# Optimization experiments

Hardware: AMD Instinct MI355X
Metric: run time of the kernel (lower is better)

The kernel has to match this reference:

```python
import jax, jax.numpy as jnp
import numpy as np
import math

PI = math.pi
PHI = (1.0 + math.sqrt(5.0)) / 2.0
D_MODEL = 1024
N_HEADS = 16
D_HEAD = D_MODEL // N_HEADS
LAYER_DEPTH = 0.5
LAYER_INDEX = 0
CONV_RATE = 0.1


def setup_inputs() -> dict:
    key = jax.random.key(0)
    ks = jax.random.split(key, 5)
    B, T = 2, 2048
    x = jax.random.normal(ks[0], (B, T, D_MODEL), dtype=jnp.float32)
    s = 1.0 / math.sqrt(D_MODEL)
    Wq = jax.random.normal(ks[1], (D_MODEL, D_MODEL), dtype=jnp.float32) * s
    Wk = jax.random.normal(ks[2], (D_MODEL, D_MODEL), dtype=jnp.float32) * s
    Wv = jax.random.normal(ks[3], (D_MODEL, D_MODEL), dtype=jnp.float32) * s
    We = jax.random.normal(ks[4], (D_MODEL, D_MODEL), dtype=jnp.float32) * s
    # per-head chamber init, matching ApertureChamber / _head_depth
    frac = jnp.arange(N_HEADS, dtype=jnp.float32) / max(N_HEADS - 1, 1)
    lo = LAYER_DEPTH * 0.5
    hi = 0.5 + LAYER_DEPTH * 0.5
    depth = lo + frac * (hi - lo)
    beta = 0.5 + 0.2 * (1.0 - 2.0 * depth)           # [H] raw (pre-sigmoid) params
    input_valve = jnp.full((N_HEADS,), 0.5, dtype=jnp.float32)
    output_valve = jnp.full((N_HEADS,), 0.5, dtype=jnp.float32)
    chi = jnp.ones((N_HEADS,), dtype=jnp.float32)
    return {"x": x, "Wq": Wq, "Wk": Wk, "Wv": Wv, "We": We,
            "beta": beta, "input_valve": input_valve,
            "output_valve": output_valve, "chi": chi}


def reference(x, Wq, Wk, Wv, We, beta, input_valve, output_valve, chi):
    B, T, D = x.shape
    H, dh = N_HEADS, D // N_HEADS
    conv_factor = 1.0 / PHI ** (LAYER_INDEX * CONV_RATE)
    scale = math.sqrt(dh * conv_factor)
    # QKV projections (torch Linear: x @ W.T), split heads -> [B,H,T,dh]
    q = (x @ Wq.T).reshape(B, T, H, dh).transpose(0, 2, 1, 3)
    k = (x @ Wk.T).reshape(B, T, H, dh).transpose(0, 2, 1, 3)
    v = (x @ Wv.T).reshape(B, T, H, dh).transpose(0, 2, 1, 3)
    attn = jax.nn.softmax(jnp.einsum('bhqd,bhkd->bhqk', q, k) / scale, axis=-1)
    converged = jnp.einsum('bhqk,bhkd->bhqd', attn, v)  # [B,H,T,dh]
    # ApertureChamber per head, vectorized over H (broadcast [H] -> [1,H,1,1])
    b = jax.nn.sigmoid(beta)[None, :, None, None]
    iv = jax.nn.sigmoid(input_valve)[None, :, None, None]
    ov = jax.nn.sigmoid(output_valve)[None, :, None, None]
    g = jnp.tanh(chi)[None, :, None, None]
    ang = PI * b
    ca, sa = jnp.cos(ang), jnp.sin(ang)
    x_in = converged * iv
    half = dh // 2  # d_head even -> no leftover lane
    xr, xi = x_in[..., :half], x_in[..., half:]
    rot = jnp.concatenate([xr * ca - xi * sa, xr * sa + xi * ca], axis=-1)
    out = rot * ov * g  # output valve + tanh(chi) gate
    combined = out.transpose(0, 2, 1, 3).reshape(B, T, D)
    return combined @ We.T
```

## Files before the change

### kernel.cpp

```cpp
#include <hip/hip_runtime.h>
#include <hip/hip_bf16.h>
#include <math.h>

typedef __bf16 bf16;
typedef __bf16 bf16x4 __attribute__((ext_vector_type(4)));
typedef __bf16 bf16x8 __attribute__((ext_vector_type(8)));
typedef float f32x4 __attribute__((ext_vector_type(4)));
typedef float f32x16 __attribute__((ext_vector_type(16)));
typedef unsigned int u32x4 __attribute__((ext_vector_type(4)));

static __device__ __forceinline__ f32x4 mfma16(bf16x8 a, bf16x8 b, f32x4 c) {
  return __builtin_amdgcn_mfma_f32_16x16x32_bf16(a, b, c, 0, 0, 0);
}
static __device__ __forceinline__ f32x16 mfma32(bf16x8 a, bf16x8 b, f32x16 c) {
  return __builtin_amdgcn_mfma_f32_32x32x16_bf16(a, b, c, 0, 0, 0);
}
static __device__ __forceinline__ void gld_lds16(const void* g, void* l) {
  __builtin_amdgcn_global_load_lds(
      (const __attribute__((address_space(1))) void*)g,
      (__attribute__((address_space(3))) void*)l, 16, 0, 0);
}
static __device__ __forceinline__ unsigned cvt_pk_bf16(float lo, float hi) {
  unsigned r;
  asm("v_cvt_pk_bf16_f32 %0, %1, %2" : "=v"(r) : "v"(lo), "v"(hi));
  return r;
}
static __device__ __forceinline__ float rsum16(f32x16 v) {
  float a0 = v[0] + v[8],  a1 = v[1] + v[9];
  float a2 = v[2] + v[10], a3 = v[3] + v[11];
  float a4 = v[4] + v[12], a5 = v[5] + v[13];
  float a6 = v[6] + v[14], a7 = v[7] + v[15];
  a0 += a4; a1 += a5; a2 += a6; a3 += a7;
  return (a0 + a1) + (a2 + a3);
}

__global__ void cast_all(const float* __restrict__ x, const float* __restrict__ Wq,
                         const float* __restrict__ Wk, const float* __restrict__ Wv,
                         const float* __restrict__ We,
                         bf16* __restrict__ xb, bf16* __restrict__ qb,
                         bf16* __restrict__ kb, bf16* __restrict__ vb,
                         bf16* __restrict__ eb) {
  int i = blockIdx.x * 256 + threadIdx.x;
  const float* s; bf16* d; int off;
  if (i < 1048576) { s = x; d = xb; off = i; }
  else {
    int j = i - 1048576; int w = j >> 18; off = j & 262143;
    s = (w == 0) ? Wq : (w == 1) ? Wk : (w == 2) ? Wv : We;
    d = (w == 0) ? qb : (w == 1) ? kb : (w == 2) ? vb : eb;
  }
  float4 v = reinterpret_cast<const float4*>(s)[off];
  bf16x4 o; o[0] = (bf16)v.x; o[1] = (bf16)v.y; o[2] = (bf16)v.z; o[3] = (bf16)v.w;
  reinterpret_cast<bf16x4*>(d)[off] = o;
}

template<int MODE>
__global__ __launch_bounds__(512, 4)
void gemm_bt(const bf16* __restrict__ A,
             const bf16* __restrict__ B0, const bf16* __restrict__ B1,
             const bf16* __restrict__ B2,
             void* __restrict__ C0v, void* __restrict__ C1v, void* __restrict__ C2v,
             int M, int N, int K) {
  __shared__ bf16 As[128 * 64];
  __shared__ bf16 Bs[128 * 64];
  const int tid = threadIdx.x;
  const int wave = tid >> 6;
  const int lane = tid & 63;
  const int bid = blockIdx.x | (blockIdx.y << 3) | (blockIdx.z << 8);
  const int cpx = gridDim.z << 5;
  const int swz = (bid & 7) * cpx + (bid >> 3);
  const int n0 = (swz & 7) * 128;
  const int m0 = ((swz >> 3) & 31) * 128;
  const int zz = swz >> 8;
  const bf16* B = (zz == 0) ? B0 : (zz == 1) ? B1 : B2;
  void* Cv = (zz == 0) ? C0v : (zz == 1) ? C1v : C2v;
  const int wr = (wave >> 1) * 32;
  const int wc = (wave & 1) * 64;
  const int frow = lane & 15;
  const int fx = frow & 7;
  const int khi = lane >> 4;
  const int srow8 = lane >> 3;
  const int scol = ((lane & 7) ^ srow8) * 8;
  f32x4 acc[2][4] = {};
  char* AsB = (char*)As;
  char* BsB = (char*)Bs;
  for (int k0 = 0; k0 < K; k0 += 64) {
    __syncthreads();
#pragma unroll
    for (int j = 0; j < 2; ++j) {
      int u = wave * 2 + j;
      int row = u * 8 + srow8;
      gld_lds16(&A[(size_t)(m0 + row) * K + k0 + scol], AsB + u * 1024);
      gld_lds16(&B[(size_t)(n0 + row) * K + k0 + scol], BsB + u * 1024);
    }
    asm volatile("s_waitcnt vmcnt(0)" ::: "memory");
    __syncthreads();
#pragma unroll
    for (int kk = 0; kk < 2; ++kk) {
      bf16x8 af[2], bfr[4];
#pragma unroll
      for (int mi = 0; mi < 2; ++mi)
        af[mi] = *reinterpret_cast<const bf16x8*>(
            AsB + (wr + mi * 16 + frow) * 128 + (((kk << 2) + khi) ^ fx) * 16);
#pragma unroll
      for (int ni = 0; ni < 4; ++ni)
        bfr[ni] = *reinterpret_cast<const bf16x8*>(
            BsB + (wc + ni * 16 + frow) * 128 + (((kk << 2) + khi) ^ fx) * 16);
      __builtin_amdgcn_s_setprio(1);
#pragma unroll
      for (int mi = 0; mi < 2; ++mi)
#pragma unroll
        for (int ni = 0; ni < 4; ++ni)
          acc[mi][ni] = mfma16(af[mi], bfr[ni], acc[mi][ni]);
      __builtin_amdgcn_s_setprio(0);
    }
  }
#pragma unroll
  for (int mi = 0; mi < 2; ++mi) {
#pragma unroll
    for (int ni = 0; ni < 4; ++ni) {
#pragma unroll
      for (int r = 0; r < 4; ++r) {
        int row = m0 + wr + mi * 16 + khi * 4 + r;
        int col = n0 + wc + ni * 16 + frow;
        if (MODE == 0) {
          int b = row >> 11, t = row & 2047, h = col >> 6, d = col & 63;
          ((bf16*)Cv)[(((size_t)b * 16 + h) * 2048 + t) * 64 + d] = (bf16)acc[mi][ni][r];
        } else {
          ((float*)Cv)[(size_t)row * N + col] = acc[mi][ni][r];
        }
      }
    }
  }
}

__global__ void transpose_v(const bf16* __restrict__ v, bf16* __restrict__ vt) {
  __shared__ bf16 tile[64][65];
  int bh = blockIdx.y;
  int t0 = blockIdx.x * 64;
  for (int idx = threadIdx.x; idx < 64 * 64; idx += 256) {
    int r = idx >> 6, c = idx & 63;
    tile[r][c] = v[((size_t)bh * 2048 + t0 + r) * 64 + c];
  }
  __syncthreads();
  for (int idx = threadIdx.x; idx < 64 * 64; idx += 256) {
    int d = idx >> 6, r = idx & 63;
    vt[((size_t)bh * 64 + d) * 2048 + t0 + r] = tile[r][d];
  }
}

__global__ __launch_bounds__(512, 4)
void attn_kernel(const bf16* __restrict__ q, const bf16* __restrict__ k,
                 const bf16* __restrict__ vt,
                 const float* __restrict__ beta, const float* __restrict__ ivp,
                 const float* __restrict__ ovp, const float* __restrict__ chip,
                 bf16* __restrict__ comb) {
  __shared__ bf16 Ks[2][2][64 * 64];
  __shared__ bf16 Vs[2][2][64 * 64];
  const int tid = threadIdx.x;
  const int wave = tid >> 6, lane = tid & 63;
  const int w4 = wave & 3, grp = wave >> 2;
  const int hi = lane >> 5, ln = lane & 31;
  const int bid = blockIdx.x | (blockIdx.y << 4);
  const int swz = (bid & 7) * 64 + (bid >> 3);
  const int qblk = swz & 15, bh = swz >> 4;
  const int h = bh & 15, b = bh >> 4;
  const int q0w = qblk * 128 + w4 * 32;
  const float C = 0.18033688011112042f;
  const float SHIFT = 28.853900817779268f;

  const bf16* qrow = q + ((size_t)bh * 2048 + q0w + ln) * 64 + hi * 8;
  bf16x8 qf[4];
#pragma unroll
  for (int ds = 0; ds < 4; ++ds)
    qf[ds] = *reinterpret_cast<const bf16x8*>(qrow + ds * 16);

  const bf16* kbase = k + (size_t)bh * 2048 * 64 + (size_t)grp * 1024 * 64;
  const bf16* vbase = vt + (size_t)bh * 64 * 2048 + grp * 1024;
  const int srow = lane >> 3;
  const int scol = ((lane & 7) ^ (srow & 7)) * 8;

  f32x16 acc0 = {}, acc1 = {};
  float lsum = 0.f;

  auto stage = [&](int buf, int k0) {
#pragma unroll
    for (int j = 0; j < 2; ++j) {
      int u = w4 * 2 + j;
      int r = u * 8 + srow;
      gld_lds16(&kbase[(size_t)(k0 + r) * 64 + scol], (char*)&Ks[grp][buf][0] + u * 1024);
      gld_lds16(&vbase[(size_t)r * 2048 + k0 + scol], (char*)&Vs[grp][buf][0] + u * 1024);
    }
  };

  stage(0, 0);
  int cur = 0;
  for (int k0 = 0; k0 < 1024; k0 += 64) {
    asm volatile("s_waitcnt vmcnt(0)" ::: "memory");
    __syncthreads();
    if (k0 + 64 < 1024) stage(cur ^ 1, k0 + 64);

    f32x16 s[2];
    s[0] = (f32x16){}; s[1] = (f32x16){};
    const char* kb = (const char*)&Ks[grp][cur][0];
    __builtin_amdgcn_s_setprio(1);
#pragma unroll
    for (int kh = 0; kh < 2; ++kh) {
      const int r = kh * 32 + ln;
      const int rx = (r & 7) << 4;
#pragma unroll
      for (int ds = 0; ds < 4; ++ds) {
        bf16x8 kf = *reinterpret_cast<const bf16x8*>(kb + r * 128 + ((ds * 32 + hi * 16) ^ rx));
        s[kh] = mfma32(kf, qf[ds], s[kh]);
      }
    }
    __builtin_amdgcn_s_setprio(0);

#pragma unroll
    for (int kh = 0; kh < 2; ++kh) {
      f32x16 z = s[kh] * C - SHIFT;
#pragma unroll
      for (int e = 0; e < 16; ++e) s[kh][e] = exp2f(z[e]);
      lsum += rsum16(s[kh]);
    }

    const char* vb = (const char*)&Vs[grp][cur][0];
#pragma unroll
    for (int ks = 0; ks < 4; ++ks) {
      const int kh = ks >> 1;
      const int b0 = 8 * (ks & 1);
      unsigned a0 = cvt_pk_bf16(s[kh][b0 + 0], s[kh][b0 + 1]);
      unsigned a1 = cvt_pk_bf16(s[kh][b0 + 4], s[kh][b0 + 5]);
      unsigned c0 = cvt_pk_bf16(s[kh][b0 + 2], s[kh][b0 + 3]);
      unsigned c1 = cvt_pk_bf16(s[kh][b0 + 6], s[kh][b0 + 7]);
      asm("v_permlane32_swap_b32 %0, %1" : "+v"(a0), "+v"(a1));
      asm("v_permlane32_swap_b32 %0, %1" : "+v"(c0), "+v"(c1));
      union { u32x4 u; bf16x8 v; } pf;
      pf.u[0] = a0; pf.u[1] = c0; pf.u[2] = a1; pf.u[3] = c1;
      __builtin_amdgcn_s_setprio(1);
#pragma unroll
      for (int dh = 0; dh < 2; ++dh) {
        const int r = dh * 32 + ln;
        bf16x8 vf = *reinterpret_cast<const bf16x8*>(
            vb + r * 128 + ((ks * 32 + hi * 16) ^ ((r & 7) << 4)));
        if (dh == 0) acc0 = mfma32(pf.v, vf, acc0);
        else         acc1 = mfma32(pf.v, vf, acc1);
      }
      __builtin_amdgcn_s_setprio(0);
    }
    cur ^= 1;
  }

  __syncthreads();
  float* exO = (float*)&Ks[0][0][0];
  float* exL = (float*)&Vs[0][0][0];
  const int xl = w4 * 64 + lane;
  if (grp == 1) {
#pragma unroll
    for (int r = 0; r < 16; ++r) {
      exO[r * 256 + xl]        = acc0[r];
      exO[(16 + r) * 256 + xl] = acc1[r];
    }
    exL[xl] = lsum;
  }
  __syncthreads();
  if (grp == 0) {
#pragma unroll
    for (int r = 0; r < 16; ++r) {
      acc0[r] += exO[r * 256 + xl];
      acc1[r] += exO[(16 + r) * 256 + xl];
    }
    lsum += exL[xl];
    lsum += __shfl_xor(lsum, 32);
    float inv = 1.f / lsum;

    float bb = 1.f / (1.f + expf(-beta[h]));
    float ang = 3.14159265358979323846f * bb;
    float ca = cosf(ang), sa = sinf(ang);
    float iv = 1.f / (1.f + expf(-ivp[h]));
    float ov = 1.f / (1.f + expf(-ovp[h]));
    float g = tanhf(chip[h]);
    float K1 = iv * ov * g * ca;
    float K2 = iv * ov * g * sa;
#pragma unroll
    for (int r = 0; r < 16; ++r) {
      int qr = (r & 3) + 8 * (r >> 2) + 4 * hi;
      float iq = __shfl(inv, qr, 32);
      float o_r = acc0[r] * iq, o_i = acc1[r] * iq;
      size_t base = ((size_t)b * 2048 + q0w + qr) * 1024 + (size_t)h * 64;
      comb[base + ln]      = (bf16)(K1 * o_r - K2 * o_i);
      comb[base + 32 + ln] = (bf16)(K2 * o_r + K1 * o_i);
    }
  }
}

extern "C" void kernel_launch(void* const* d_in, const int* in_sizes, int n_in,
                              void* d_out, int out_size, void* d_ws, size_t ws_size,
                              hipStream_t stream) {
  const float* x    = (const float*)d_in[0];
  const float* Wq   = (const float*)d_in[1];
  const float* Wk   = (const float*)d_in[2];
  const float* Wv   = (const float*)d_in[3];
  const float* We   = (const float*)d_in[4];
  const float* beta = (const float*)d_in[5];
  const float* ivp  = (const float*)d_in[6];
  const float* ovp  = (const float*)d_in[7];
  const float* chip = (const float*)d_in[8];

  char* ws = (char*)d_ws;
  bf16* x_bf  = (bf16*)(ws + (size_t)0);
  bf16* Wq_bf = (bf16*)(ws + ((size_t)8  << 20));
  bf16* Wk_bf = (bf16*)(ws + ((size_t)10 << 20));
  bf16* Wv_bf = (bf16*)(ws + ((size_t)12 << 20));
  bf16* We_bf = (bf16*)(ws + ((size_t)14 << 20));
  bf16* q_bf  = (bf16*)(ws + ((size_t)16 << 20));
  bf16* k_bf  = (bf16*)(ws + ((size_t)24 << 20));
  bf16* v_bf  = (bf16*)(ws + ((size_t)32 << 20));
  bf16* v_t   = (bf16*)(ws + ((size_t)40 << 20));
  bf16* comb  = (bf16*)(ws + ((size_t)48 << 20));

  cast_all<<<8192, 256, 0, stream>>>(x, Wq, Wk, Wv, We, x_bf, Wq_bf, Wk_bf, Wv_bf, We_bf);

  gemm_bt<0><<<dim3(8, 32, 3), 512, 0, stream>>>(x_bf, Wq_bf, Wk_bf, Wv_bf,
                                                 q_bf, k_bf, v_bf, 4096, 1024, 1024);
  transpose_v<<<dim3(32, 32), 256, 0, stream>>>(v_bf, v_t);
  attn_kernel<<<dim3(16, 32), 512, 0, stream>>>(q_bf, k_bf, v_t, beta, ivp, ovp, chip, comb);
  gemm_bt<1><<<dim3(8, 32, 1), 512, 0, stream>>>(comb, We_bf, We_bf, We_bf,
                                                 d_out, d_out, d_out, 4096, 1024, 1024);
}
```

Before: 198.2 us.

## Restructure attention into 3-way key split with 64-query blocks and 6 waves

The attention kernel now processes 64 queries per block across 6 waves: 2 query slices times 3 key slices of 704/704/640 keys. Each slice runs 32-key tiles and stages V every other iteration, with single-buffered LDS and two barriers per tile instead of double buffering. Partial outputs from the three key slices are reduced through LDS at the end. The goal is more blocks (1024) and higher occupancy to raise parallelism, at the cost of losing load/compute overlap and adding more barriers and smaller MFMA batches per tile.

```diff
diff --git a/kernel.cpp b/kernel.cpp
--- a/kernel.cpp
+++ b/kernel.cpp
@@ -148,128 +148,122 @@
   }
 }
 
-__global__ __launch_bounds__(512, 4)
+__global__ __launch_bounds__(384, 6)
 void attn_kernel(const bf16* __restrict__ q, const bf16* __restrict__ k,
                  const bf16* __restrict__ vt,
                  const float* __restrict__ beta, const float* __restrict__ ivp,
                  const float* __restrict__ ovp, const float* __restrict__ chip,
                  bf16* __restrict__ comb) {
-  __shared__ bf16 Ks[2][2][64 * 64];
-  __shared__ bf16 Vs[2][2][64 * 64];
+  __shared__ char lds[36864];
   const int tid = threadIdx.x;
   const int wave = tid >> 6, lane = tid & 63;
-  const int w4 = wave & 3, grp = wave >> 2;
+  const int qs = wave & 1, sl = wave >> 1;
   const int hi = lane >> 5, ln = lane & 31;
-  const int bid = blockIdx.x | (blockIdx.y << 4);
-  const int swz = (bid & 7) * 64 + (bid >> 3);
-  const int qblk = swz & 15, bh = swz >> 4;
+  const int bid = blockIdx.x | (blockIdx.y << 5);
+  const int swz = (bid & 7) * 128 + (bid >> 3);
+  const int qblk = swz & 31, bh = swz >> 5;
   const int h = bh & 15, b = bh >> 4;
-  const int q0w = qblk * 128 + w4 * 32;
+  const int q0w = qblk * 64 + qs * 32;
   const float C = 0.18033688011112042f;
   const float SHIFT = 28.853900817779268f;
 
+  const int kb0 = sl * 704;
+  const int ntile = (sl == 2) ? 20 : 22;
+
   const bf16* qrow = q + ((size_t)bh * 2048 + q0w + ln) * 64 + hi * 8;
   bf16x8 qf[4];
 #pragma unroll
   for (int ds = 0; ds < 4; ++ds)
     qf[ds] = *reinterpret_cast<const bf16x8*>(qrow + ds * 16);
 
-  const bf16* kbase = k + (size_t)bh * 2048 * 64 + (size_t)grp * 1024 * 64;
-  const bf16* vbase = vt + (size_t)bh * 64 * 2048 + grp * 1024;
+  const bf16* kbase = k + (size_t)bh * 2048 * 64;
+  const bf16* vbase = vt + (size_t)bh * 64 * 2048;
   const int srow = lane >> 3;
-  const int scol = ((lane & 7) ^ (srow & 7)) * 8;
+  const int scol = ((lane & 7) ^ srow) * 8;
+  char* Ksl = lds + sl * 12288;
+  char* Vsl = Ksl + 4096;
 
   f32x16 acc0 = {}, acc1 = {};
   float lsum = 0.f;
 
-  auto stage = [&](int buf, int k0) {
-#pragma unroll
-    for (int j = 0; j < 2; ++j) {
-      int u = w4 * 2 + j;
-      int r = u * 8 + srow;
-      gld_lds16(&kbase[(size_t)(k0 + r) * 64 + scol], (char*)&Ks[grp][buf][0] + u * 1024);
-      gld_lds16(&vbase[(size_t)r * 2048 + k0 + scol], (char*)&Vs[grp][buf][0] + u * 1024);
-    }
-  };
-
-  stage(0, 0);
-  int cur = 0;
-  for (int k0 = 0; k0 < 1024; k0 += 64) {
+  for (int i = 0; i < 22; ++i) {
+    const bool g = (i < ntile);
+    if (g) {
+#pragma unroll
+      for (int j = 0; j < 2; ++j) {
+        int u = qs * 2 + j;
+        int key = kb0 + i * 32 + u * 8 + srow;
+        gld_lds16(&kbase[(size_t)key * 64 + scol], Ksl + u * 1024);
+      }
+      if (!(i & 1)) {
+#pragma unroll
+        for (int j = 0; j < 4; ++j) {
+          int u = qs * 4 + j;
+          int d = u * 8 + srow;
+          gld_lds16(&vbase[(size_t)d * 2048 + kb0 + i * 32 + scol], Vsl + u * 1024);
+        }
+      }
+    }
     asm volatile("s_waitcnt vmcnt(0)" ::: "memory");
     __syncthreads();
-    if (k0 + 64 < 1024) stage(cur ^ 1, k0 + 64);
-
-    f32x16 s[2];
-    s[0] = (f32x16){}; s[1] = (f32x16){};
-    const char* kb = (const char*)&Ks[grp][cur][0];
-    __builtin_amdgcn_s_setprio(1);
-#pragma unroll
-    for (int kh = 0; kh < 2; ++kh) {
-      const int r = kh * 32 + ln;
-      const int rx = (r & 7) << 4;
+    if (g) {
+      f32x16 s = {};
+      __builtin_amdgcn_s_setprio(1);
 #pragma unroll
       for (int ds = 0; ds < 4; ++ds) {
-        bf16x8 kf = *reinterpret_cast<const bf16x8*>(kb + r * 128 + ((ds * 32 + hi * 16) ^ rx));
-        s[kh] = mfma32(kf, qf[ds], s[kh]);
-      }
-    }
-    __builtin_amdgcn_s_setprio(0);
-
-#pragma unroll
-    for (int kh = 0; kh < 2; ++kh) {
-      f32x16 z = s[kh] * C - SHIFT;
-#pragma unroll
-      for (int e = 0; e < 16; ++e) s[kh][e] = exp2f(z[e]);
-      lsum += rsum16(s[kh]);
-    }
-
-    const char* vb = (const char*)&Vs[grp][cur][0];
-#pragma unroll
-    for (int ks = 0; ks < 4; ++ks) {
-      const int kh = ks >> 1;
-      const int b0 = 8 * (ks & 1);
-      unsigned a0 = cvt_pk_bf16(s[kh][b0 + 0], s[kh][b0 + 1]);
-      unsigned a1 = cvt_pk_bf16(s[kh][b0 + 4], s[kh][b0 + 5]);
-      unsigned c0 = cvt_pk_bf16(s[kh][b0 + 2], s[kh][b0 + 3]);
-      unsigned c1 = cvt_pk_bf16(s[kh][b0 + 6], s[kh][b0 + 7]);
-      asm("v_permlane32_swap_b32 %0, %1" : "+v"(a0), "+v"(a1));
-      asm("v_permlane32_swap_b32 %0, %1" : "+v"(c0), "+v"(c1));
-      union { u32x4 u; bf16x8 v; } pf;
-      pf.u[0] = a0; pf.u[1] = c0; pf.u[2] = a1; pf.u[3] = c1;
-      __builtin_amdgcn_s_setprio(1);
-#pragma unroll
-      for (int dh = 0; dh < 2; ++dh) {
-        const int r = dh * 32 + ln;
-        bf16x8 vf = *reinterpret_cast<const bf16x8*>(
-            vb + r * 128 + ((ks * 32 + hi * 16) ^ ((r & 7) << 4)));
-        if (dh == 0) acc0 = mfma32(pf.v, vf, acc0);
-        else         acc1 = mfma32(pf.v, vf, acc1);
+        bf16x8 kf = *reinterpret_cast<const bf16x8*>(
+            Ksl + ln * 128 + (((ds * 2 + hi) ^ (ln & 7)) * 16));
+        s = mfma32(kf, qf[ds], s);
       }
       __builtin_amdgcn_s_setprio(0);
-    }
-    cur ^= 1;
-  }
-
+#pragma unroll
+      for (int e = 0; e < 16; ++e) s[e] = exp2f(fmaf(s[e], C, -SHIFT));
+      lsum += rsum16(s);
+#pragma unroll
+      for (int ks = 0; ks < 2; ++ks) {
+        const int b0 = 8 * ks;
+        unsigned a0 = cvt_pk_bf16(s[b0 + 0], s[b0 + 1]);
+        unsigned a1 = cvt_pk_bf16(s[b0 + 4], s[b0 + 5]);
+        unsigned c0 = cvt_pk_bf16(s[b0 + 2], s[b0 + 3]);
+        unsigned c1 = cvt_pk_bf16(s[b0 + 6], s[b0 + 7]);
+        asm("v_permlane32_swap_b32 %0, %1" : "+v"(a0), "+v"(a1));
+        asm("v_permlane32_swap_b32 %0, %1" : "+v"(c0), "+v"(c1));
+        union { u32x4 u; bf16x8 v; } pf;
+        pf.u[0] = a0; pf.u[1] = c0; pf.u[2] = a1; pf.u[3] = c1;
+        __builtin_amdgcn_s_setprio(1);
+#pragma unroll
+        for (int dh = 0; dh < 2; ++dh) {
+          const int r = dh * 32 + ln;
+          bf16x8 vf = *reinterpret_cast<const bf16x8*>(
+              Vsl + r * 128 + ((((i & 1) * 4 + ks * 2 + hi) ^ (r & 7)) * 16));
+          if (dh == 0) acc0 = mfma32(pf.v, vf, acc0);
+          else         acc1 = mfma32(pf.v, vf, acc1);
+        }
+        __builtin_amdgcn_s_setprio(0);
+      }
+    }
+    __syncthreads();
+  }
+
+  float* scr = (float*)lds;
+  if (sl > 0) {
+    const int seg = ((sl - 1) * 2 + qs) * 2112;
+#pragma unroll
+    for (int r = 0; r < 16; ++r) {
+      scr[seg + r * 64 + lane]        = acc0[r];
+      scr[seg + 1024 + r * 64 + lane] = acc1[r];
+    }
+    scr[seg + 2048 + lane] = lsum;
+  }
   __syncthreads();
-  float* exO = (float*)&Ks[0][0][0];
-  float* exL = (float*)&Vs[0][0][0];
-  const int xl = w4 * 64 + lane;
-  if (grp == 1) {
+  if (sl == 0) {
+    const int s1 = qs * 2112, s2 = (2 + qs) * 2112;
 #pragma unroll
     for (int r = 0; r < 16; ++r) {
-      exO[r * 256 + xl]        = acc0[r];
-      exO[(16 + r) * 256 + xl] = acc1[r];
-    }
-    exL[xl] = lsum;
-  }
-  __syncthreads();
-  if (grp == 0) {
-#pragma unroll
-    for (int r = 0; r < 16; ++r) {
-      acc0[r] += exO[r * 256 + xl];
-      acc1[r] += exO[(16 + r) * 256 + xl];
-    }
-    lsum += exL[xl];
+      acc0[r] += scr[s1 + r * 64 + lane] + scr[s2 + r * 64 + lane];
+      acc1[r] += scr[s1 + 1024 + r * 64 + lane] + scr[s2 + 1024 + r * 64 + lane];
+    }
+    lsum += scr[s1 + 2048 + lane] + scr[s2 + 2048 + lane];
     lsum += __shfl_xor(lsum, 32);
     float inv = 1.f / lsum;
 
@@ -323,7 +317,7 @@
   gemm_bt<0><<<dim3(8, 32, 3), 512, 0, stream>>>(x_bf, Wq_bf, Wk_bf, Wv_bf,
                                                  q_bf, k_bf, v_bf, 4096, 1024, 1024);
   transpose_v<<<dim3(32, 32), 256, 0, stream>>>(v_bf, v_t);
-  attn_kernel<<<dim3(16, 32), 512, 0, stream>>>(q_bf, k_bf, v_t, beta, ivp, ovp, chip, comb);
+  attn_kernel<<<dim3(32, 32), 384, 0, stream>>>(q_bf, k_bf, v_t, beta, ivp, ovp, chip, comb);
   gemm_bt<1><<<dim3(8, 32, 1), 512, 0, stream>>>(comb, We_bf, We_bf, We_bf,
                                                  d_out, d_out, d_out, 4096, 1024, 1024);
 }
```

After: 287.0 us. 44.8% more time.
